# Kernel tuning notes

Measured on AMD Instinct MI355X. Metric: run time of the kernel, lower is better.

The kernel has to match this reference:

```python
import jax, jax.numpy as jnp
import numpy as np

H = 16        # num_attention_heads
D = 1024      # hidden_size
HD = D // H   # head_dim = 64


def setup_inputs() -> dict:
    key = jax.random.key(0)
    ks = jax.random.split(key, 5)
    B, T = 16, 1024
    s_in = 1.0 / np.sqrt(D)
    return {
        "hidden_states": jax.random.normal(ks[0], (B, T, D), dtype=jnp.float32),
        "w_qkv": jax.random.normal(ks[1], (D, 3 * D), dtype=jnp.float32) * s_in,
        "b_qkv": jnp.zeros((3 * D,), dtype=jnp.float32),
        "w_out": jax.random.normal(ks[2], (D, D), dtype=jnp.float32) * s_in,
        "b_out": jnp.zeros((D,), dtype=jnp.float32),
    }


def reference(hidden_states, w_qkv, b_qkv, w_out, b_out):
    B, T, C = hidden_states.shape
    qkv = hidden_states @ w_qkv + b_qkv                      # [B,T,3C]
    q, k, v = jnp.split(qkv, 3, axis=-1)
    # [B,T,C] -> [B,H,T,HD]
    q = q.reshape(B, T, H, HD).transpose(0, 2, 1, 3)
    k = k.reshape(B, T, H, HD).transpose(0, 2, 1, 3)
    v = v.reshape(B, T, H, HD).transpose(0, 2, 1, 3)
    scale = 1.0 / np.sqrt(HD)
    logits = jnp.einsum("bhqd,bhkd->bhqk", q, k) * scale     # [B,H,T,T]
    attn = jax.nn.softmax(logits, axis=-1)
    out = jnp.einsum("bhqk,bhkd->bhqd", attn, v)             # [B,H,T,HD]
    out = out.transpose(0, 2, 1, 3).reshape(B, T, C)
    return out @ w_out + b_out
```

## Files before the change

kernel.cpp:

```cpp
#include <hip/hip_runtime.h>
#include <cstdint>
#include <cstddef>

typedef _Float16 h8 __attribute__((ext_vector_type(8)));
typedef _Float16 h4 __attribute__((ext_vector_type(4)));
typedef __fp16 fp16x2 __attribute__((ext_vector_type(2)));
typedef float f4 __attribute__((ext_vector_type(4)));

#define MFMA(a, b, c) __builtin_amdgcn_mfma_f32_16x16x32_f16((a), (b), (c), 0, 0, 0)

__device__ __forceinline__ void gl_lds16(const void* g, void* l) {
  __builtin_amdgcn_global_load_lds((const __attribute__((address_space(1))) void*)g,
                                   (__attribute__((address_space(3))) void*)l, 16, 0, 0);
}

__device__ __forceinline__ h8 lds_frag(const char* base, int r, int ch) {
  return *(const h8*)(base + ((r * 8 + (ch ^ (r & 7))) * 16));
}

__device__ __forceinline__ void BAR() {
  asm volatile("" ::: "memory");
  __builtin_amdgcn_s_barrier();
  asm volatile("" ::: "memory");
}

__global__ void k_cvt_hs(const float* __restrict__ in, _Float16* __restrict__ out, int n8) {
  int i = blockIdx.x * blockDim.x + threadIdx.x;
  if (i >= n8) return;
  size_t idx = (size_t)i * 8;
  float4 a = *(const float4*)(in + idx);
  float4 b = *(const float4*)(in + idx + 4);
  h8 o;
  o[0] = (_Float16)a.x; o[1] = (_Float16)a.y; o[2] = (_Float16)a.z; o[3] = (_Float16)a.w;
  o[4] = (_Float16)b.x; o[5] = (_Float16)b.y; o[6] = (_Float16)b.z; o[7] = (_Float16)b.w;
  *(h8*)(out + idx) = o;
}

__global__ void k_transcvt(const float* __restrict__ in, _Float16* __restrict__ out, int N, int K) {
  __shared__ float tile[64 * 65];
  int tn = blockIdx.x * 64, tk = blockIdx.y * 64;
  for (int i = 0; i < 4; ++i) {
    int cid = i * 256 + threadIdx.x;
    int r = cid >> 4, c4 = cid & 15;
    float4 v = *(const float4*)(in + (size_t)(tk + r) * N + tn + c4 * 4);
    tile[r * 65 + c4 * 4 + 0] = v.x; tile[r * 65 + c4 * 4 + 1] = v.y;
    tile[r * 65 + c4 * 4 + 2] = v.z; tile[r * 65 + c4 * 4 + 3] = v.w;
  }
  __syncthreads();
  for (int i = 0; i < 2; ++i) {
    int cid = i * 256 + threadIdx.x;
    int n = cid >> 3, kc = cid & 7;
    h8 o;
    for (int j = 0; j < 8; ++j) o[j] = (_Float16)tile[(kc * 8 + j) * 65 + n];
    *(h8*)(out + (size_t)(tn + n) * K + tk + kc * 8) = o;
  }
}

__device__ __forceinline__ void gemm256_tile(
    const _Float16* __restrict__ Ab, const _Float16* __restrict__ Bb,
    const _Float16* __restrict__ BbN, bool first, bool more,
    char* smem, f4 (&acc)[8][4]) {
  constexpr int TILE = 32768, HALF = 16384;
  int tid = threadIdx.x, lane = tid & 63, wave = tid >> 6;
  int l15 = lane & 15, l4 = lane >> 4;
  int wm = (wave >> 2) * 128, wn = (wave & 3) * 64;
  int rs = tid >> 3, cg = (tid & 7) ^ (rs & 7);
  char* cA = smem;            char* nA = smem + TILE;
  char* cB = smem + 2 * TILE; char* nB = smem + 3 * TILE;

  auto stA = [&](int kt, int h, char* dst) {
    const _Float16* s = Ab + (size_t)(h * 128 + rs) * 1024 + kt + cg * 8;
    gl_lds16(s, dst + h * HALF + tid * 16);
    gl_lds16(s + (size_t)64 * 1024, dst + h * HALF + 8192 + tid * 16);
  };
  auto stB = [&](const _Float16* base, int kt, int h, char* dst) {
    const _Float16* s = base + (size_t)(h * 128 + rs) * 1024 + kt + cg * 8;
    gl_lds16(s, dst + h * HALF + tid * 16);
    gl_lds16(s + (size_t)64 * 1024, dst + h * HALF + 8192 + tid * 16);
  };

  if (first) {
    stA(0, 0, cA); stA(0, 1, cA);
    stB(Bb, 0, 0, cB); stB(Bb, 0, 1, cB);
    stB(Bb, 64, 0, nB); stB(Bb, 64, 1, nB);
    asm volatile("s_waitcnt vmcnt(4)" ::: "memory");
    BAR();
  }

  h8 af[4][2], bf[4][2];
  for (int u = 0; u < 16; ++u) {
    int kt1 = (u + 1) << 6, kt2 = (u + 2) << 6;
#pragma unroll
    for (int mi = 0; mi < 4; ++mi) {
      int r = wm + mi * 16 + l15;
      af[mi][0] = lds_frag(cA, r, l4);
      af[mi][1] = lds_frag(cA, r, 4 + l4);
    }
#pragma unroll
    for (int nj = 0; nj < 2; ++nj) {
      int r = wn + nj * 16 + l15;
      bf[nj][0] = lds_frag(cB, r, l4);
      bf[nj][1] = lds_frag(cB, r, 4 + l4);
    }
    if (u < 15) stA(kt1, 0, nA);
    else if (more) stA(0, 0, nA);
    asm volatile("s_waitcnt lgkmcnt(8)" ::: "memory");
    BAR();
    asm volatile("s_waitcnt lgkmcnt(0)" ::: "memory");
    __builtin_amdgcn_s_setprio(1);
#pragma unroll
    for (int kk = 0; kk < 2; ++kk)
#pragma unroll
      for (int mi = 0; mi < 4; ++mi)
#pragma unroll
        for (int nj = 0; nj < 2; ++nj)
          acc[mi][nj] = MFMA(af[mi][kk], bf[nj][kk], acc[mi][nj]);
    __builtin_amdgcn_s_setprio(0);
    BAR();
#pragma unroll
    for (int nj = 2; nj < 4; ++nj) {
      int r = wn + nj * 16 + l15;
      bf[nj][0] = lds_frag(cB, r, l4);
      bf[nj][1] = lds_frag(cB, r, 4 + l4);
    }
    if (u < 15) stA(kt1, 1, nA);
    else if (more) stA(0, 1, nA);
    BAR();
    asm volatile("s_waitcnt lgkmcnt(0)" ::: "memory");
    __builtin_amdgcn_s_setprio(1);
#pragma unroll
    for (int kk = 0; kk < 2; ++kk)
#pragma unroll
      for (int mi = 0; mi < 4; ++mi)
#pragma unroll
        for (int nj = 2; nj < 4; ++nj)
          acc[mi][nj] = MFMA(af[mi][kk], bf[nj][kk], acc[mi][nj]);
    __builtin_amdgcn_s_setprio(0);
    BAR();
#pragma unroll
    for (int mi = 0; mi < 4; ++mi) {
      int r = wm + 64 + mi * 16 + l15;
      af[mi][0] = lds_frag(cA, r, l4);
      af[mi][1] = lds_frag(cA, r, 4 + l4);
    }
    if (u < 14) stB(Bb, kt2, 0, cB);
    else if (more) stB(BbN, (u == 14) ? 0 : 64, 0, cB);
    BAR();
    asm volatile("s_waitcnt lgkmcnt(0)" ::: "memory");
    __builtin_amdgcn_s_setprio(1);
#pragma unroll
    for (int kk = 0; kk < 2; ++kk)
#pragma unroll
      for (int mi = 0; mi < 4; ++mi)
#pragma unroll
        for (int nj = 2; nj < 4; ++nj)
          acc[4 + mi][nj] = MFMA(af[mi][kk], bf[nj][kk], acc[4 + mi][nj]);
    __builtin_amdgcn_s_setprio(0);
    BAR();
    if (u < 14) stB(Bb, kt2, 1, cB);
    else if (more) stB(BbN, (u == 14) ? 0 : 64, 1, cB);
    if (u < 14 || more) asm volatile("s_waitcnt vmcnt(4)" ::: "memory");
    else                asm volatile("s_waitcnt vmcnt(0)" ::: "memory");
    BAR();
    __builtin_amdgcn_s_setprio(1);
#pragma unroll
    for (int kk = 0; kk < 2; ++kk)
#pragma unroll
      for (int mi = 0; mi < 4; ++mi)
#pragma unroll
        for (int nj = 0; nj < 2; ++nj)
          acc[4 + mi][nj] = MFMA(af[mi][kk], bf[nj][kk], acc[4 + mi][nj]);
    __builtin_amdgcn_s_setprio(0);
    BAR();
    char* t = cA; cA = nA; nA = t;
    t = cB; cB = nB; nB = t;
  }
}

__global__ __launch_bounds__(512) void k_gemm_qkv(
    const _Float16* __restrict__ A, const _Float16* __restrict__ BT,
    const float* __restrict__ bias,
    _Float16* __restrict__ Q, _Float16* __restrict__ Kq, _Float16* __restrict__ Vt) {
  __shared__ char smem[131072];
  int id = blockIdx.x;
  int swz = (id & 7) * 32 + (id >> 3);
  int by = swz >> 2, c = swz & 3;
  int tm = by * 256;
  const _Float16* Ab = A + (size_t)tm * 1024;
  int tid = threadIdx.x, lane = tid & 63, wave = tid >> 6;
  int l15 = lane & 15, l4 = lane >> 4;
  int wm = (wave >> 2) * 128, wn = (wave & 3) * 64;

  for (int t = 0; t < 3; ++t) {
    int tn = (t * 4 + c) * 256;
    const _Float16* Bb = BT + (size_t)tn * 1024;
    const _Float16* BbN = Bb + (size_t)1024 * 1024;
    f4 acc[8][4] = {};
    gemm256_tile(Ab, Bb, BbN, t == 0, t < 2, smem, acc);

    if (t < 2) {
      _Float16* dst = (t == 0) ? Q : Kq;
#pragma unroll
      for (int nj = 0; nj < 4; ++nj) {
        int n = tn + wn + nj * 16 + l15;
        float bv = bias[n];
        int h = (n >> 6) & 15, d = n & 63;
#pragma unroll
        for (int mig = 0; mig < 8; ++mig) {
#pragma unroll
          for (int r = 0; r < 4; ++r) {
            int m = tm + wm + mig * 16 + l4 * 4 + r;
            int b = m >> 10, tt = m & 1023;
            dst[(((size_t)b * 16 + h) * 1024 + tt) * 64 + d] =
                (_Float16)(acc[mig][nj][r] + bv);
          }
        }
      }
    } else {
      _Float16* L = (_Float16*)smem;
      int b = tm >> 10, tb = tm & 1023;
#pragma unroll
      for (int p = 0; p < 2; ++p) {
        __syncthreads();
        if (((wave >> 1) & 1) == p) {
          int nloc = (wave & 1) * 64;
#pragma unroll
          for (int nj = 0; nj < 4; ++nj) {
            int nl = nloc + nj * 16 + l15;
            float bv = bias[tn + p * 128 + nl];
#pragma unroll
            for (int mig = 0; mig < 8; ++mig) {
              h4 pk;
#pragma unroll
              for (int r = 0; r < 4; ++r) pk[r] = (_Float16)(acc[mig][nj][r] + bv);
              *(h4*)(L + nl * 264 + wm + mig * 16 + l4 * 4) = pk;
            }
          }
        }
        __syncthreads();
#pragma unroll
        for (int i = 0; i < 8; ++i) {
          int cid = i * 512 + tid;
          int nl = cid >> 5, tc = cid & 31;
          int ng = tn + p * 128 + nl;
          int h = (ng >> 6) & 15, d = ng & 63;
          *(h8*)(Vt + (((size_t)b * 16 + h) * 64 + d) * 1024 + tb + tc * 8) =
              *(const h8*)(L + nl * 264 + tc * 8);
        }
      }
    }
  }
}

__global__ __launch_bounds__(256, 2) void k_attn(
    const _Float16* __restrict__ Q, const _Float16* __restrict__ Kk,
    const _Float16* __restrict__ Vt, _Float16* __restrict__ O) {
  __shared__ char smem[20480 + 32768];
  _Float16* sP = (_Float16*)smem;
  char* sKV = smem + 20480;
  const float SCL = 0.125f * 1.44269504088896340736f;
  int tid = threadIdx.x, wave = tid >> 6, lane = tid & 63;
  int l15 = lane & 15, l4 = lane >> 4;
  int bh = blockIdx.y;
  int qt = blockIdx.x * 256;
  const _Float16* Qb = Q + (size_t)bh * 65536;
  const _Float16* Kb = Kk + (size_t)bh * 65536;
  const _Float16* Vb = Vt + (size_t)bh * 65536;

  h8 qf[4][2];
#pragma unroll
  for (int nt = 0; nt < 4; ++nt) {
    int r = qt + wave * 64 + nt * 16 + l15;
#pragma unroll
    for (int kk = 0; kk < 2; ++kk)
      qf[nt][kk] = *(const h8*)(Qb + (size_t)r * 64 + (kk * 4 + l4) * 8);
  }
  _Float16 scl_h = (_Float16)SCL;
#pragma unroll
  for (int nt = 0; nt < 4; ++nt)
#pragma unroll
    for (int kk = 0; kk < 2; ++kk)
#pragma unroll
      for (int j = 0; j < 8; ++j) qf[nt][kk][j] *= scl_h;

  int cid0 = tid, cid1 = tid + 256;
  int r0 = cid0 >> 3, c0 = (cid0 & 7) ^ (r0 & 7);
  int r1 = cid1 >> 3, c1 = (cid1 & 7) ^ (r1 & 7);
  const _Float16* kp0 = Kb + (size_t)r0 * 64 + c0 * 8;
  const _Float16* kp1 = Kb + (size_t)r1 * 64 + c1 * 8;
  const _Float16* vp0 = Vb + (size_t)r0 * 1024 + c0 * 8;
  const _Float16* vp1 = Vb + (size_t)r1 * 1024 + c1 * 8;

  auto stage = [&](int it, int b) {
    char* dK = sKV + b * 16384;
    char* dV = dK + 8192;
    size_t ko = (size_t)it * 4096;
    size_t vo = (size_t)it * 64;
    gl_lds16(kp0 + ko, dK + cid0 * 16);
    gl_lds16(kp1 + ko, dK + cid1 * 16);
    gl_lds16(vp0 + vo, dV + cid0 * 16);
    gl_lds16(vp1 + vo, dV + cid1 * 16);
  };

  f4 oacc[4][4] = {};
  f4 lacc[4] = {};
  h8 ones;
#pragma unroll
  for (int j = 0; j < 8; ++j) ones[j] = (_Float16)1.0f;
  _Float16* pw = sP + wave * 64 * 40;

  stage(0, 0);
  asm volatile("s_waitcnt vmcnt(0)" ::: "memory");
  BAR();

  for (int it = 0; it < 16; ++it) {
    int cur = it & 1;
    if (it < 15) stage(it + 1, cur ^ 1);
    const char* sK = sKV + cur * 16384;
    const char* sV = sK + 8192;
    for (int mh = 0; mh < 2; ++mh) {
      f4 sacc[2][4] = {};
#pragma unroll
      for (int kk = 0; kk < 2; ++kk) {
        h8 kf[2];
        int ch = kk * 4 + l4;
#pragma unroll
        for (int mt = 0; mt < 2; ++mt) {
          int r = mh * 32 + mt * 16 + l15;
          kf[mt] = *(const h8*)(sK + ((r * 8 + (ch ^ (r & 7))) * 16));
        }
#pragma unroll
        for (int mt = 0; mt < 2; ++mt)
#pragma unroll
          for (int nt = 0; nt < 4; ++nt)
            sacc[mt][nt] = MFMA(kf[mt], qf[nt][kk], sacc[mt][nt]);
      }
#pragma unroll
      for (int mt = 0; mt < 2; ++mt) {
#pragma unroll
        for (int nt = 0; nt < 4; ++nt) {
          float p0 = __builtin_amdgcn_exp2f(sacc[mt][nt][0]);
          float p1 = __builtin_amdgcn_exp2f(sacc[mt][nt][1]);
          float p2 = __builtin_amdgcn_exp2f(sacc[mt][nt][2]);
          float p3 = __builtin_amdgcn_exp2f(sacc[mt][nt][3]);
          union { fp16x2 h[2]; h4 v; } uu;
          uu.h[0] = __builtin_amdgcn_cvt_pkrtz(p0, p1);
          uu.h[1] = __builtin_amdgcn_cvt_pkrtz(p2, p3);
          *(h4*)(pw + (nt * 16 + l15) * 40 + mt * 16 + l4 * 4) = uu.v;
        }
      }
      h8 pf[4], vf[4];
#pragma unroll
      for (int mi = 0; mi < 4; ++mi)
        pf[mi] = *(const h8*)(pw + (mi * 16 + l15) * 40 + l4 * 8);
      int ch = mh * 4 + l4;
#pragma unroll
      for (int nd = 0; nd < 4; ++nd) {
        int r = nd * 16 + l15;
        vf[nd] = *(const h8*)(sV + ((r * 8 + (ch ^ (r & 7))) * 16));
      }
#pragma unroll
      for (int mi = 0; mi < 4; ++mi) {
#pragma unroll
        for (int nd = 0; nd < 4; ++nd)
          oacc[mi][nd] = MFMA(pf[mi], vf[nd], oacc[mi][nd]);
        lacc[mi] = MFMA(pf[mi], ones, lacc[mi]);
      }
    }
    asm volatile("s_waitcnt vmcnt(0)" ::: "memory");
    BAR();
  }
  int b = bh >> 4, h = bh & 15;
#pragma unroll
  for (int mi = 0; mi < 4; ++mi) {
#pragma unroll
    for (int r = 0; r < 4; ++r) {
      float inv = 1.f / lacc[mi][r];
      int t = qt + wave * 64 + mi * 16 + l4 * 4 + r;
#pragma unroll
      for (int nd = 0; nd < 4; ++nd)
        O[(size_t)(b * 1024 + t) * 1024 + h * 64 + nd * 16 + l15] =
            (_Float16)(oacc[mi][nd][r] * inv);
    }
  }
}

__global__ __launch_bounds__(512) void k_gemm_out(
    const _Float16* __restrict__ A, const _Float16* __restrict__ BT,
    const float* __restrict__ bias, float* __restrict__ C) {
  __shared__ char smem[131072];
  int id = blockIdx.x;
  int swz = (id & 7) * 32 + (id >> 3);
  int by = swz >> 2, bx = swz & 3;
  int tm = by * 256, tn = bx * 256;
  f4 acc[8][4] = {};
  gemm256_tile(A + (size_t)tm * 1024, BT + (size_t)tn * 1024, nullptr,
               true, false, smem, acc);

  int tid = threadIdx.x, lane = tid & 63, wave = tid >> 6;
  int l15 = lane & 15, l4 = lane >> 4;
  int wm = (wave >> 2) * 128, wn = (wave & 3) * 64;
#pragma unroll
  for (int nj = 0; nj < 4; ++nj) {
    int n = tn + wn + nj * 16 + l15;
    float bv = bias[n];
#pragma unroll
    for (int mig = 0; mig < 8; ++mig) {
#pragma unroll
      for (int r = 0; r < 4; ++r) {
        int m = tm + wm + mig * 16 + l4 * 4 + r;
        C[(size_t)m * 1024 + n] = acc[mig][nj][r] + bv;
      }
    }
  }
}

extern "C" void kernel_launch(void* const* d_in, const int* in_sizes, int n_in,
                              void* d_out, int out_size, void* d_ws, size_t ws_size,
                              hipStream_t stream) {
  const float* hs    = (const float*)d_in[0];
  const float* w_qkv = (const float*)d_in[1];
  const float* b_qkv = (const float*)d_in[2];
  const float* w_out = (const float*)d_in[3];
  const float* b_out = (const float*)d_in[4];
  float* out = (float*)d_out;
  char* ws = (char*)d_ws;

  _Float16* hs_h  = (_Float16*)(ws);
  _Float16* wqkvT = (_Float16*)(ws + 33554432);
  _Float16* woutT = (_Float16*)(ws + 39845888);
  _Float16* q_ws  = (_Float16*)(ws + 41943040);
  _Float16* k_ws  = (_Float16*)(ws + 75497472);
  _Float16* vt_ws = (_Float16*)(ws + 109051904);

  k_cvt_hs<<<8192, 256, 0, stream>>>(hs, hs_h, 2097152);
  k_transcvt<<<dim3(48, 16), 256, 0, stream>>>(w_qkv, wqkvT, 3072, 1024);
  k_transcvt<<<dim3(16, 16), 256, 0, stream>>>(w_out, woutT, 1024, 1024);
  k_gemm_qkv<<<256, 512, 0, stream>>>(hs_h, wqkvT, b_qkv, q_ws, k_ws, vt_ws);
  _Float16* attn_h = hs_h;
  k_attn<<<dim3(4, 256), 256, 0, stream>>>(q_ws, k_ws, vt_ws, attn_h);
  k_gemm_out<<<256, 512, 0, stream>>>(attn_h, woutT, b_out, out);
}
```

Before: 359.2 us.

## Fuse fp32-to-fp16 hidden state conversion into QKV GEMM A-tile staging

Removes the standalone conversion kernel for hidden_states and has the QKV GEMM load fp32 A tiles into registers, convert to fp16, and write them to LDS after the last MFMA block of each iteration. This eliminates a full write and re-read of the fp16 copy and one kernel launch. In exchange, A staging no longer uses direct global-to-LDS loads, adds register pressure and in-loop conversion work, and reads twice as many bytes per A tile, which is repeated across the three N passes.

```diff
diff --git a/kernel.cpp b/kernel.cpp
--- a/kernel.cpp
+++ b/kernel.cpp
@@ -22,18 +22,6 @@
   asm volatile("" ::: "memory");
   __builtin_amdgcn_s_barrier();
   asm volatile("" ::: "memory");
-}
-
-__global__ void k_cvt_hs(const float* __restrict__ in, _Float16* __restrict__ out, int n8) {
-  int i = blockIdx.x * blockDim.x + threadIdx.x;
-  if (i >= n8) return;
-  size_t idx = (size_t)i * 8;
-  float4 a = *(const float4*)(in + idx);
-  float4 b = *(const float4*)(in + idx + 4);
-  h8 o;
-  o[0] = (_Float16)a.x; o[1] = (_Float16)a.y; o[2] = (_Float16)a.z; o[3] = (_Float16)a.w;
-  o[4] = (_Float16)b.x; o[5] = (_Float16)b.y; o[6] = (_Float16)b.z; o[7] = (_Float16)b.w;
-  *(h8*)(out + idx) = o;
 }
 
 __global__ void k_transcvt(const float* __restrict__ in, _Float16* __restrict__ out, int N, int K) {
@@ -56,10 +44,11 @@
   }
 }
 
+template <bool A32>
 __device__ __forceinline__ void gemm256_tile(
-    const _Float16* __restrict__ Ab, const _Float16* __restrict__ Bb,
-    const _Float16* __restrict__ BbN, bool first, bool more,
-    char* smem, f4 (&acc)[8][4]) {
+    const _Float16* __restrict__ Ab, const float* __restrict__ Af,
+    const _Float16* __restrict__ Bb, const _Float16* __restrict__ BbN,
+    bool first, bool more, char* smem, f4 (&acc)[8][4]) {
   constexpr int TILE = 32768, HALF = 16384;
   int tid = threadIdx.x, lane = tid & 63, wave = tid >> 6;
   int l15 = lane & 15, l4 = lane >> 4;
@@ -68,10 +57,30 @@
   char* cA = smem;            char* nA = smem + TILE;
   char* cB = smem + 2 * TILE; char* nB = smem + 3 * TILE;
 
-  auto stA = [&](int kt, int h, char* dst) {
+  auto stA16 = [&](int kt, int h, char* dst) {
     const _Float16* s = Ab + (size_t)(h * 128 + rs) * 1024 + kt + cg * 8;
     gl_lds16(s, dst + h * HALF + tid * 16);
     gl_lds16(s + (size_t)64 * 1024, dst + h * HALF + 8192 + tid * 16);
+  };
+  auto ldA32 = [&](int kt, int h, float4 (&v)[4]) {
+    const float* s = Af + (size_t)(h * 128 + rs) * 1024 + kt + cg * 8;
+    v[0] = *(const float4*)(s);
+    v[1] = *(const float4*)(s + 4);
+    v[2] = *(const float4*)(s + (size_t)64 * 1024);
+    v[3] = *(const float4*)(s + (size_t)64 * 1024 + 4);
+  };
+  auto wrA32 = [&](char* dst, int h, float4 (&v)[4]) {
+    h8 o0, o1;
+    o0[0] = (_Float16)v[0].x; o0[1] = (_Float16)v[0].y;
+    o0[2] = (_Float16)v[0].z; o0[3] = (_Float16)v[0].w;
+    o0[4] = (_Float16)v[1].x; o0[5] = (_Float16)v[1].y;
+    o0[6] = (_Float16)v[1].z; o0[7] = (_Float16)v[1].w;
+    o1[0] = (_Float16)v[2].x; o1[1] = (_Float16)v[2].y;
+    o1[2] = (_Float16)v[2].z; o1[3] = (_Float16)v[2].w;
+    o1[4] = (_Float16)v[3].x; o1[5] = (_Float16)v[3].y;
+    o1[6] = (_Float16)v[3].z; o1[7] = (_Float16)v[3].w;
+    *(h8*)(dst + h * HALF + tid * 16) = o0;
+    *(h8*)(dst + h * HALF + 8192 + tid * 16) = o1;
   };
   auto stB = [&](const _Float16* base, int kt, int h, char* dst) {
     const _Float16* s = base + (size_t)(h * 128 + rs) * 1024 + kt + cg * 8;
@@ -79,17 +88,31 @@
     gl_lds16(s + (size_t)64 * 1024, dst + h * HALF + 8192 + tid * 16);
   };
 
+  float4 a0[4], a1[4];
+
   if (first) {
-    stA(0, 0, cA); stA(0, 1, cA);
-    stB(Bb, 0, 0, cB); stB(Bb, 0, 1, cB);
-    stB(Bb, 64, 0, nB); stB(Bb, 64, 1, nB);
-    asm volatile("s_waitcnt vmcnt(4)" ::: "memory");
+    if constexpr (A32) {
+      ldA32(0, 0, a0); ldA32(0, 1, a1);
+      stB(Bb, 0, 0, cB); stB(Bb, 0, 1, cB);
+      stB(Bb, 64, 0, nB); stB(Bb, 64, 1, nB);
+      asm volatile("s_waitcnt vmcnt(8)" ::: "memory");
+      wrA32(cA, 0, a0); wrA32(cA, 1, a1);
+      asm volatile("s_waitcnt lgkmcnt(0)" ::: "memory");
+      asm volatile("s_waitcnt vmcnt(4)" ::: "memory");
+    } else {
+      stA16(0, 0, cA); stA16(0, 1, cA);
+      stB(Bb, 0, 0, cB); stB(Bb, 0, 1, cB);
+      stB(Bb, 64, 0, nB); stB(Bb, 64, 1, nB);
+      asm volatile("s_waitcnt vmcnt(4)" ::: "memory");
+    }
     BAR();
   }
 
   h8 af[4][2], bf[4][2];
   for (int u = 0; u < 16; ++u) {
     int kt1 = (u + 1) << 6, kt2 = (u + 2) << 6;
+    bool stage_a = (u < 15) || more;
+    int akt = (u < 15) ? kt1 : 0;
 #pragma unroll
     for (int mi = 0; mi < 4; ++mi) {
       int r = wm + mi * 16 + l15;
@@ -102,8 +125,10 @@
       bf[nj][0] = lds_frag(cB, r, l4);
       bf[nj][1] = lds_frag(cB, r, 4 + l4);
     }
-    if (u < 15) stA(kt1, 0, nA);
-    else if (more) stA(0, 0, nA);
+    if (stage_a) {
+      if constexpr (A32) ldA32(akt, 0, a0);
+      else stA16(akt, 0, nA);
+    }
     asm volatile("s_waitcnt lgkmcnt(8)" ::: "memory");
     BAR();
     asm volatile("s_waitcnt lgkmcnt(0)" ::: "memory");
@@ -123,8 +148,10 @@
       bf[nj][0] = lds_frag(cB, r, l4);
       bf[nj][1] = lds_frag(cB, r, 4 + l4);
     }
-    if (u < 15) stA(kt1, 1, nA);
-    else if (more) stA(0, 1, nA);
+    if (stage_a) {
+      if constexpr (A32) ldA32(akt, 1, a1);
+      else stA16(akt, 1, nA);
+    }
     BAR();
     asm volatile("s_waitcnt lgkmcnt(0)" ::: "memory");
     __builtin_amdgcn_s_setprio(1);
@@ -171,6 +198,12 @@
         for (int nj = 0; nj < 2; ++nj)
           acc[4 + mi][nj] = MFMA(af[mi][kk], bf[nj][kk], acc[4 + mi][nj]);
     __builtin_amdgcn_s_setprio(0);
+    if constexpr (A32) {
+      if (stage_a) {
+        wrA32(nA, 0, a0); wrA32(nA, 1, a1);
+        asm volatile("s_waitcnt lgkmcnt(0)" ::: "memory");
+      }
+    }
     BAR();
     char* t = cA; cA = nA; nA = t;
     t = cB; cB = nB; nB = t;
@@ -178,7 +211,7 @@
 }
 
 __global__ __launch_bounds__(512) void k_gemm_qkv(
-    const _Float16* __restrict__ A, const _Float16* __restrict__ BT,
+    const float* __restrict__ A32, const _Float16* __restrict__ BT,
     const float* __restrict__ bias,
     _Float16* __restrict__ Q, _Float16* __restrict__ Kq, _Float16* __restrict__ Vt) {
   __shared__ char smem[131072];
@@ -186,7 +219,7 @@
   int swz = (id & 7) * 32 + (id >> 3);
   int by = swz >> 2, c = swz & 3;
   int tm = by * 256;
-  const _Float16* Ab = A + (size_t)tm * 1024;
+  const float* Af = A32 + (size_t)tm * 1024;
   int tid = threadIdx.x, lane = tid & 63, wave = tid >> 6;
   int l15 = lane & 15, l4 = lane >> 4;
   int wm = (wave >> 2) * 128, wn = (wave & 3) * 64;
@@ -196,7 +229,7 @@
     const _Float16* Bb = BT + (size_t)tn * 1024;
     const _Float16* BbN = Bb + (size_t)1024 * 1024;
     f4 acc[8][4] = {};
-    gemm256_tile(Ab, Bb, BbN, t == 0, t < 2, smem, acc);
+    gemm256_tile<true>(nullptr, Af, Bb, BbN, t == 0, t < 2, smem, acc);
 
     if (t < 2) {
       _Float16* dst = (t == 0) ? Q : Kq;
@@ -394,8 +427,8 @@
   int by = swz >> 2, bx = swz & 3;
   int tm = by * 256, tn = bx * 256;
   f4 acc[8][4] = {};
-  gemm256_tile(A + (size_t)tm * 1024, BT + (size_t)tn * 1024, nullptr,
-               true, false, smem, acc);
+  gemm256_tile<false>(A + (size_t)tm * 1024, nullptr, BT + (size_t)tn * 1024,
+                      nullptr, true, false, smem, acc);
 
   int tid = threadIdx.x, lane = tid & 63, wave = tid >> 6;
   int l15 = lane & 15, l4 = lane >> 4;
@@ -426,18 +459,16 @@
   float* out = (float*)d_out;
   char* ws = (char*)d_ws;
 
-  _Float16* hs_h  = (_Float16*)(ws);
+  _Float16* attn_h = (_Float16*)(ws);
   _Float16* wqkvT = (_Float16*)(ws + 33554432);
   _Float16* woutT = (_Float16*)(ws + 39845888);
   _Float16* q_ws  = (_Float16*)(ws + 41943040);
   _Float16* k_ws  = (_Float16*)(ws + 75497472);
   _Float16* vt_ws = (_Float16*)(ws + 109051904);
 
-  k_cvt_hs<<<8192, 256, 0, stream>>>(hs, hs_h, 2097152);
   k_transcvt<<<dim3(48, 16), 256, 0, stream>>>(w_qkv, wqkvT, 3072, 1024);
   k_transcvt<<<dim3(16, 16), 256, 0, stream>>>(w_out, woutT, 1024, 1024);
-  k_gemm_qkv<<<256, 512, 0, stream>>>(hs_h, wqkvT, b_qkv, q_ws, k_ws, vt_ws);
-  _Float16* attn_h = hs_h;
+  k_gemm_qkv<<<256, 512, 0, stream>>>(hs, wqkvT, b_qkv, q_ws, k_ws, vt_ws);
   k_attn<<<dim3(4, 256), 256, 0, stream>>>(q_ws, k_ws, vt_ws, attn_h);
   k_gemm_out<<<256, 512, 0, stream>>>(attn_h, woutT, b_out, out);
 }
```

After: 414.1 us. +15.3%, slower.
